# Optimization experiments

Measured on AMD Instinct MI355X. Metric: run time of the kernel, lower is better.

Reference implementation:

```python
import jax, jax.numpy as jnp
import numpy as np

N = 20000
E = 500000
NS = 128
NT = 128
BN_EPS = 1e-3
DIMS = [NS, 2 * NT, 4 * NT, 2 * NT, NT, NT]


def setup_inputs() -> dict:
    key = jax.random.key(0)
    ks = jax.random.split(key, 32)
    inp = {
        "x": jax.random.normal(ks[0], (N, NS), jnp.float32),
        "edge_index": jax.random.randint(ks[1], (2, E), 0, N),
        "edge_attr": jax.random.uniform(ks[2], (E,), jnp.float32),
    }
    for i in range(5):
        din, dout = DIMS[i], DIMS[i + 1]
        inp[f"W{i+1}"] = jax.random.normal(ks[3 + i], (din, dout), jnp.float32) * (1.0 / np.sqrt(din)).astype(np.float32)
        inp[f"b{i+1}"] = jnp.zeros((dout,), jnp.float32)
    for i in range(4):
        d = DIMS[i + 1]
        inp[f"g{i+1}"] = 1.0 + 0.1 * jax.random.normal(ks[10 + i], (d,), jnp.float32)
        inp[f"be{i+1}"] = 0.1 * jax.random.normal(ks[14 + i], (d,), jnp.float32)
        inp[f"m{i+1}"] = 0.1 * jax.random.normal(ks[18 + i], (d,), jnp.float32)
        inp[f"v{i+1}"] = jax.random.uniform(ks[22 + i], (d,), jnp.float32, minval=0.5, maxval=1.5)
    return inp


def gcn_norm(edge_index, edge_attr, n):
    # PyG gcn_norm with self-loops (fill value 1) and symmetric degree norm.
    loop = jnp.arange(n)
    row = jnp.concatenate([edge_index[0], loop])
    col = jnp.concatenate([edge_index[1], loop])
    w = jnp.concatenate([edge_attr, jnp.ones((n,), edge_attr.dtype)])
    deg = jax.ops.segment_sum(w, col, num_segments=n)
    dinv = jnp.where(deg > 0, jax.lax.rsqrt(deg), 0.0)
    return row, col, dinv[row] * w * dinv[col]


def gcn_conv(h, W, b, row, col, norm, n):
    # out[col] += norm * (h @ W)[row]; then add bias (PyG GCNConv).
    hw = h @ W
    agg = jax.ops.segment_sum(hw[row] * norm[:, None], col, num_segments=n)
    return agg + b


def bn_eval(h, g, be, m, v):
    return (h - m) * jax.lax.rsqrt(v + BN_EPS) * g + be


def reference(x, edge_index, edge_attr,
              W1, b1, W2, b2, W3, b3, W4, b4, W5, b5,
              g1, be1, m1, v1, g2, be2, m2, v2,
              g3, be3, m3, v3, g4, be4, m4, v4):
    n = x.shape[0]
    row, col, norm = gcn_norm(edge_index, edge_attr, n)  # cached=True: shared by all layers
    h = jax.nn.sigmoid(bn_eval(gcn_conv(x, W1, b1, row, col, norm, n), g1, be1, m1, v1))
    h = jax.nn.sigmoid(bn_eval(gcn_conv(h, W2, b2, row, col, norm, n), g2, be2, m2, v2))
    h = jax.nn.sigmoid(bn_eval(gcn_conv(h, W3, b3, row, col, norm, n), g3, be3, m3, v3))
    h = jax.nn.sigmoid(bn_eval(gcn_conv(h, W4, b4, row, col, norm, n), g4, be4, m4, v4))
    h = jax.nn.sigmoid(gcn_conv(h, W5, b5, row, col, norm, n))
    # dropout is identity in eval mode
    x11 = h.T @ h  # [NT, NT]
    x12 = 0.5 * (x11 + x11.T)
    return x12 - jnp.diag(jnp.diag(x12))
```

## Files before the change

kernel.cpp:

```cpp
#include <hip/hip_runtime.h>
#include <hip/hip_bf16.h>
#include <hip/hip_fp8.h>
#include <cstdint>
#include <cstddef>

typedef __hip_bfloat16 bf16;
typedef unsigned char fp8;
typedef __attribute__((ext_vector_type(8))) short short8;
typedef __attribute__((ext_vector_type(4))) float f32x4;
typedef __attribute__((ext_vector_type(2))) float f32x2;

#define NSF 128
#define BN_EPS 1e-3f
#define NR 4
#define SCK 2048


__global__ void zero_fill_kernel(int* __restrict__ fill, int total) {
    int i = blockIdx.x * blockDim.x + threadIdx.x;
    if (i < total) fill[i] = 0;
}

__global__ void passA_kernel(const int* __restrict__ ei, int* __restrict__ fill,
                             int* __restrict__ loc, int E, int n, int rsize) {
    int idx = blockIdx.x * blockDim.x + threadIdx.x;
    if (idx < E) {
        int r = ei[idx];
        int c = ei[E + idx];
        int slot = c * NR + r / rsize;
        loc[idx] = atomicAdd(&fill[slot], 1);
    } else if (idx < E + n) {
        int i = idx - E;
        int slot = i * NR + i / rsize;
        loc[idx] = atomicAdd(&fill[slot], 1);
    }
}


__global__ void scan1_kernel(const int* __restrict__ cnt, int* __restrict__ blksum, int total) {
    __shared__ int red[256];
    int base = blockIdx.x * SCK + threadIdx.x * 8;
    int s = 0;
    #pragma unroll
    for (int i = 0; i < 8; ++i) {
        int idx = base + i;
        if (idx < total) s += cnt[idx];
    }
    red[threadIdx.x] = s;
    __syncthreads();
    for (int off2 = 128; off2 > 0; off2 >>= 1) {
        if (threadIdx.x < off2) red[threadIdx.x] += red[threadIdx.x + off2];
        __syncthreads();
    }
    if (threadIdx.x == 0) blksum[blockIdx.x] = red[0];
}

__global__ void scan2_kernel(int* __restrict__ blksum, int* __restrict__ row_ptr,
                             int nblk, int total) {
    __shared__ int part[256];
    int tid = threadIdx.x;
    int v = (tid < nblk) ? blksum[tid] : 0;
    part[tid] = v;
    __syncthreads();
    for (int off2 = 1; off2 < 256; off2 <<= 1) {
        int t = (tid >= off2) ? part[tid - off2] : 0;
        __syncthreads();
        part[tid] += t;
        __syncthreads();
    }
    if (tid < nblk) blksum[tid] = part[tid] - v;
    if (tid == 255) row_ptr[total] = part[255];
}

__global__ void scan3_kernel(const int* __restrict__ cnt, const int* __restrict__ blkoff,
                             int* __restrict__ row_ptr, int total) {
    __shared__ int part[256];
    int tid = threadIdx.x;
    int base = blockIdx.x * SCK + tid * 8;
    int loc[8]; int s = 0;
    #pragma unroll
    for (int i = 0; i < 8; ++i) {
        int idx = base + i;
        loc[i] = (idx < total) ? cnt[idx] : 0;
        s += loc[i];
    }
    part[tid] = s;
    __syncthreads();
    for (int off2 = 1; off2 < 256; off2 <<= 1) {
        int t = (tid >= off2) ? part[tid - off2] : 0;
        __syncthreads();
        part[tid] += t;
        __syncthreads();
    }
    int run = blkoff[blockIdx.x] + part[tid] - s;
    #pragma unroll
    for (int i = 0; i < 8; ++i) {
        int idx = base + i;
        if (idx < total) { row_ptr[idx] = run; run += loc[i]; }
    }
}

__global__ void passB_kernel(const int* __restrict__ ei, const float* __restrict__ ea,
                             const int* __restrict__ row_ptr, const int* __restrict__ loc,
                             int2* __restrict__ e8, int* __restrict__ csr_col,
                             int E, int n, int rsize) {
    int idx = blockIdx.x * blockDim.x + threadIdx.x;
    if (idx < E) {
        int r = ei[idx];
        int c = ei[E + idx];
        int slot = c * NR + r / rsize;
        int p = row_ptr[slot] + loc[idx];
        int2 rec; rec.x = r; rec.y = __float_as_int(ea[idx]);
        e8[p] = rec;
        csr_col[p] = c;
    } else if (idx < E + n) {
        int i = idx - E;
        int slot = i * NR + i / rsize;
        int p = row_ptr[slot] + loc[idx];
        int2 rec; rec.x = i; rec.y = __float_as_int(1.0f);
        e8[p] = rec;
        csr_col[p] = i;
    }
}

__global__ void degdinv_kernel(const int* __restrict__ row_ptr, const int2* __restrict__ e8,
                               float* __restrict__ dinv, int n) {
    int node = blockIdx.x * blockDim.x + threadIdx.x;
    if (node < n) {
        int s = row_ptr[node * NR], e = row_ptr[(node + 1) * NR];
        float d = 0.0f;
        for (int j = s; j < e; ++j) d += __int_as_float(e8[j].y);
        dinv[node] = (d > 0.0f) ? rsqrtf(d) : 0.0f;
    }
}

__global__ void normw_kernel(const float* __restrict__ dinv, const int* __restrict__ csr_col,
                             int2* __restrict__ e8, int EN) {
    int p = blockIdx.x * blockDim.x + threadIdx.x;
    if (p < EN) {
        int2 rec = e8[p];
        float w = dinv[rec.x] * __int_as_float(rec.y) * dinv[csr_col[p]];
        ((int*)e8)[2 * p + 1] = __float_as_int(w);
    }
}


__device__ inline void store_val(bf16* C, size_t idx, float a) {
    C[idx] = __float2bfloat16(a);
}
__device__ inline void store_val(fp8* C, size_t idx, float a) {
    int packed = __builtin_amdgcn_cvt_pk_fp8_f32(a, a, 0, false);
    C[idx] = (fp8)(packed & 0xff);
}

__global__ void prep_kernel(const float* __restrict__ x, fp8* __restrict__ xq, int xcnt,
                            const float* __restrict__ W0, const float* __restrict__ W1,
                            const float* __restrict__ W2, const float* __restrict__ W3,
                            const float* __restrict__ W4,
                            bf16* __restrict__ wtbuf, int wtelems) {
    int idx = blockIdx.x * blockDim.x + threadIdx.x;
    if (idx < xcnt) {
        store_val(xq, idx, x[idx]);
        return;
    }
    int widx = idx - xcnt;
    if (widx >= wtelems) return;
    const float* W; int K, N, off;
    if (widx < 32768)       { W = W0; K = 128; N = 256; off = 0; }
    else if (widx < 163840) { W = W1; K = 256; N = 512; off = 32768; }
    else if (widx < 294912) { W = W2; K = 512; N = 256; off = 163840; }
    else if (widx < 327680) { W = W3; K = 256; N = 128; off = 294912; }
    else                    { W = W4; K = 128; N = 128; off = 327680; }
    int l = widx - off;
    int nn = l / K, kk = l % K;
    wtbuf[widx] = __float2bfloat16(W[(size_t)kk * N + nn]);
}


__device__ inline void gl_lds16(const bf16* g, bf16* l) {
    __builtin_amdgcn_global_load_lds(
        (const __attribute__((address_space(1))) void*)g,
        (__attribute__((address_space(3))) void*)l,
        16, 0, 0);
}


template <typename OT>
__global__ __launch_bounds__(256) void mfma_gemm_kernel(
    const bf16* __restrict__ A, const bf16* __restrict__ Wt,
    OT* __restrict__ C, int M, int K, int N, int mode,
    const float* __restrict__ bias, const float* __restrict__ g,
    const float* __restrict__ be, const float* __restrict__ m,
    const float* __restrict__ v) {
    __shared__ bf16 As[64][32];
    __shared__ bf16 Bs[128][32];
    int m0 = blockIdx.x * 64;
    int n0 = blockIdx.y * 128;
    int tid = threadIdx.x;
    int wave = tid >> 6, lane = tid & 63;
    int lrow = lane & 15, quad = lane >> 4;

    f32x4 acc[8] = {};

    int srow = lane >> 2;
    int sseg = lane & 3;
    int am = wave * 16 + srow;
    int bn = wave * 32 + srow;
    bool aok = (m0 + am) < M;

    for (int k0 = 0; k0 < K; k0 += 32) {
        if (aok)
            gl_lds16(A + (size_t)(m0 + am) * K + k0 + sseg * 8, &As[am][sseg * 8]);
        gl_lds16(Wt + (size_t)(n0 + bn) * K + k0 + sseg * 8, &Bs[bn][sseg * 8]);
        gl_lds16(Wt + (size_t)(n0 + bn + 16) * K + k0 + sseg * 8, &Bs[bn + 16][sseg * 8]);
        __syncthreads();

        short8 afrag = *(const short8*)(&As[wave * 16 + lrow][quad * 8]);
        #pragma unroll
        for (int t = 0; t < 8; ++t) {
            short8 bfrag = *(const short8*)(&Bs[t * 16 + lrow][quad * 8]);
            acc[t] = __builtin_amdgcn_mfma_f32_16x16x32_bf16(afrag, bfrag, acc[t], 0, 0, 0);
        }
        __syncthreads();
    }
    #pragma unroll
    for (int t = 0; t < 8; ++t) {
        int gn = n0 + t * 16 + lrow;
        float bsc = 0.0f, scale = 1.0f, mean = 0.0f, beta = 0.0f;
        if (mode == 1) {
            bsc = bias[gn];
            scale = g[gn] * rsqrtf(v[gn] + BN_EPS);
            mean = m[gn];
            beta = be[gn];
        }
        #pragma unroll
        for (int rr = 0; rr < 4; ++rr) {
            int gm = m0 + wave * 16 + quad * 4 + rr;
            if (gm < M) {
                float a = acc[t][rr];
                if (mode == 1) {
                    a = (a + bsc - mean) * scale + beta;
                    a = 1.0f / (1.0f + __expf(-a));
                }
                store_val(C, (size_t)gm * N + gn, a);
            }
        }
    }
}


template <int VEC> struct F8Vec;
template <> struct F8Vec<2> { typedef unsigned short T; };
template <> struct F8Vec<4> { typedef unsigned int T; };

__device__ inline void fma_f8(unsigned short q, float w, float* acc) {
    f32x2 lo = __builtin_amdgcn_cvt_pk_f32_fp8((unsigned int)q, false);
    acc[0] += w * lo.x;
    acc[1] += w * lo.y;
}
__device__ inline void fma_f8(unsigned int q, float w, float* acc) {
    f32x2 lo = __builtin_amdgcn_cvt_pk_f32_fp8(q, false);
    f32x2 hi = __builtin_amdgcn_cvt_pk_f32_fp8(q, true);
    acc[0] += w * lo.x;
    acc[1] += w * lo.y;
    acc[2] += w * hi.x;
    acc[3] += w * hi.y;
}

template <int VEC>
__global__ __launch_bounds__(256) void agg_fp8_kernel(
    const fp8* __restrict__ hw,
    const int* __restrict__ row_ptr, const int2* __restrict__ e8,
    const float* __restrict__ bias,
    const float* __restrict__ g, const float* __restrict__ be,
    const float* __restrict__ m, const float* __restrict__ v,
    bf16* __restrict__ out, int n, int mode) {
    typedef typename F8Vec<VEC>::T T;
    const int dfeat = VEC * 64;
    int wave = threadIdx.x >> 6;
    int lane = threadIdx.x & 63;
    int node = blockIdx.x * 4 + wave;
    if (node >= n) return;
    int s = row_ptr[node * NR], e = row_ptr[(node + 1) * NR];
    float acc[VEC];
    #pragma unroll
    for (int i = 0; i < VEC; ++i) acc[i] = 0.0f;
    const size_t base = (size_t)lane * VEC;

    int j = s;
    for (; j + 7 < e; j += 8) {
        int2 ew[8];
        #pragma unroll
        for (int u = 0; u < 8; ++u) ew[u] = e8[j + u];
        T q[8];
        #pragma unroll
        for (int u = 0; u < 8; ++u)
            q[u] = *(const T*)(hw + (size_t)ew[u].x * dfeat + base);
        #pragma unroll
        for (int u = 0; u < 8; ++u)
            fma_f8(q[u], __int_as_float(ew[u].y), acc);
    }
    for (; j + 3 < e; j += 4) {
        int2 ew[4];
        #pragma unroll
        for (int u = 0; u < 4; ++u) ew[u] = e8[j + u];
        T q[4];
        #pragma unroll
        for (int u = 0; u < 4; ++u)
            q[u] = *(const T*)(hw + (size_t)ew[u].x * dfeat + base);
        #pragma unroll
        for (int u = 0; u < 4; ++u)
            fma_f8(q[u], __int_as_float(ew[u].y), acc);
    }
    for (; j < e; ++j) {
        int2 ew = e8[j];
        T q = *(const T*)(hw + (size_t)ew.x * dfeat + base);
        fma_f8(q, __int_as_float(ew.y), acc);
    }

    #pragma unroll
    for (int i = 0; i < VEC; ++i) {
        int f = (int)base + i;
        float a = acc[i];
        if (mode != 0) {
            a += bias[f];
            if (mode == 1) {
                float scale = g[f] * rsqrtf(v[f] + BN_EPS);
                a = (a - m[f]) * scale + be[f];
            }
            a = 1.0f / (1.0f + __expf(-a));
        }
        out[(size_t)node * dfeat + f] = __float2bfloat16(a);
    }
}

#define TPAD 8

__global__ __launch_bounds__(256) void htht_mfma_kernel(
    const bf16* __restrict__ h, float* __restrict__ partial, int n) {
    __shared__ bf16 hsT[128][32 + TPAD];
    int b = blockIdx.x;
    int tid = threadIdx.x;
    int wave = tid >> 6, lane = tid & 63;
    int lrow = lane & 15, quad = lane >> 4;

    f32x4 acc[2][8] = {};

    int kk = tid >> 3;
    int seg = tid & 7;

    for (int kt = 0; kt < 8; ++kt) {
        int k0 = b * 256 + kt * 32;
        #pragma unroll
        for (int s2 = 0; s2 < 2; ++s2) {
            int fs = (seg + s2 * 8) * 8;
            int gk = k0 + kk;
            uint4 q; q.x = q.y = q.z = q.w = 0u;
            if (gk < n) q = *(const uint4*)(h + (size_t)gk * 128 + fs);
            const unsigned short* u = (const unsigned short*)&q;
            #pragma unroll
            for (int i = 0; i < 8; ++i)
                *((unsigned short*)&hsT[fs + i][kk]) = u[i];
        }
        __syncthreads();
        short8 af0 = *(const short8*)(&hsT[wave * 32 + lrow][quad * 8]);
        short8 af1 = *(const short8*)(&hsT[wave * 32 + 16 + lrow][quad * 8]);
        #pragma unroll
        for (int t = 0; t < 8; ++t) {
            short8 bfrag = *(const short8*)(&hsT[t * 16 + lrow][quad * 8]);
            acc[0][t] = __builtin_amdgcn_mfma_f32_16x16x32_bf16(af0, bfrag, acc[0][t], 0, 0, 0);
            acc[1][t] = __builtin_amdgcn_mfma_f32_16x16x32_bf16(af1, bfrag, acc[1][t], 0, 0, 0);
        }
        __syncthreads();
    }
    float* p = partial + (size_t)b * 16384;
    #pragma unroll
    for (int a_ = 0; a_ < 2; ++a_) {
        #pragma unroll
        for (int t = 0; t < 8; ++t) {
            #pragma unroll
            for (int rr = 0; rr < 4; ++rr) {
                int gm = wave * 32 + a_ * 16 + quad * 4 + rr;
                int gn = t * 16 + lrow;
                p[gm * 128 + gn] = acc[a_][t][rr];
            }
        }
    }
}

__global__ void reduce_kernel(const float* __restrict__ partial, float* __restrict__ out, int nchunks) {
    int idx = blockIdx.x * blockDim.x + threadIdx.x;
    float s = 0.0f;
    for (int c = 0; c < nchunks; ++c) s += partial[(size_t)c * 16384 + idx];
    int i = idx / 128, j = idx % 128;
    out[idx] = (i == j) ? 0.0f : s;
}

extern "C" void kernel_launch(void* const* d_in, const int* in_sizes, int n_in,
                              void* d_out, int out_size, void* d_ws, size_t ws_size,
                              hipStream_t stream) {
    const float* x  = (const float*)d_in[0];
    const int*   ei = (const int*)d_in[1];
    const float* ea = (const float*)d_in[2];
    const float* W[5];  const float* bvec[5];
    for (int l = 0; l < 5; ++l) { W[l] = (const float*)d_in[3 + 2 * l]; bvec[l] = (const float*)d_in[4 + 2 * l]; }
    const float* g[4]; const float* be[4]; const float* mm[4]; const float* vv[4];
    for (int l = 0; l < 4; ++l) {
        g[l]  = (const float*)d_in[13 + 4 * l];
        be[l] = (const float*)d_in[14 + 4 * l];
        mm[l] = (const float*)d_in[15 + 4 * l];
        vv[l] = (const float*)d_in[16 + 4 * l];
    }
    const int n = in_sizes[0] / NSF;
    const int E = in_sizes[1] / 2;
    const int EN = E + n;
    const int rsize = (n + NR - 1) / NR;
    const int total = n * NR;
    const int nscan = (total + SCK - 1) / SCK;
    const int dims[6] = {128, 256, 512, 256, 128, 128};
    const int wtoff[5] = {0, 32768, 163840, 294912, 327680};
    const int wtelems = 344064;

    auto align = [](size_t o) { return (o + 255) & ~(size_t)255; };
    size_t off = 0;
    float* dinv    = (float*)((char*)d_ws + off); off = align(off + (size_t)n * 4);
    int*   fill    = (int*)  ((char*)d_ws + off); off = align(off + (size_t)total * 4);
    int*   row_ptr = (int*)  ((char*)d_ws + off); off = align(off + ((size_t)total + 1) * 4);
    int*   blksum  = (int*)  ((char*)d_ws + off); off = align(off + (size_t)256 * 4);
    int*   locb    = (int*)  ((char*)d_ws + off); off = align(off + (size_t)EN * 4);
    int2*  e8      = (int2*) ((char*)d_ws + off); off = align(off + (size_t)EN * 8);
    int*   csr_col = (int*)  ((char*)d_ws + off); off = align(off + (size_t)EN * 4);
    bf16*  wtbuf   = (bf16*) ((char*)d_ws + off); off = align(off + (size_t)wtelems * 2);
    fp8*   xq      = (fp8*)  ((char*)d_ws + off); off = align(off + (size_t)n * 128);
    bf16*  hbuf    = (bf16*) ((char*)d_ws + off); off = align(off + (size_t)n * 512 * 2);
    bf16*  abuf    = (bf16*) ((char*)d_ws + off); off = align(off + (size_t)n * 512 * 2);
    fp8*   f8buf   = (fp8*)  ((char*)d_ws + off); off = align(off + (size_t)n * 256);
    const int KCH = (20000 + 255) / 256;
    float* partial = (float*)((char*)d_ws + off); off = align(off + (size_t)KCH * 16384 * 4);

    zero_fill_kernel<<<(total + 255) / 256, 256, 0, stream>>>(fill, total);
    passA_kernel<<<(EN + 255) / 256, 256, 0, stream>>>(ei, fill, locb, E, n, rsize);
    scan1_kernel<<<nscan, 256, 0, stream>>>(fill, blksum, total);
    scan2_kernel<<<1, 256, 0, stream>>>(blksum, row_ptr, nscan, total);
    scan3_kernel<<<nscan, 256, 0, stream>>>(fill, blksum, row_ptr, total);
    passB_kernel<<<(EN + 255) / 256, 256, 0, stream>>>(ei, ea, row_ptr, locb,
                                                       e8, csr_col, E, n, rsize);
    degdinv_kernel<<<(n + 255) / 256, 256, 0, stream>>>(row_ptr, e8, dinv, n);
    normw_kernel<<<(EN + 255) / 256, 256, 0, stream>>>(dinv, csr_col, e8, EN);

    {
        int xcnt = n * 128;
        int items = xcnt + wtelems;
        prep_kernel<<<(items + 255) / 256, 256, 0, stream>>>(x, xq, xcnt,
            W[0], W[1], W[2], W[3], W[4], wtbuf, wtelems);
    }

    int ablocks = (n + 3) / 4;
    auto gemm_bf16 = [&](const bf16* A, int l, bf16* C, int mode) {
        int K = dims[l], N = dims[l + 1];
        dim3 gg((n + 63) / 64, N / 128);
        int bi = (l < 4) ? l : 0;
        mfma_gemm_kernel<bf16><<<gg, 256, 0, stream>>>(A, wtbuf + wtoff[l], C, n, K, N, mode,
                                                       bvec[l], g[bi], be[bi], mm[bi], vv[bi]);
    };
    auto gemm_fp8 = [&](const bf16* A, int l, fp8* C, int mode) {
        int K = dims[l], N = dims[l + 1];
        dim3 gg((n + 63) / 64, N / 128);
        int bi = (l < 4) ? l : 0;
        mfma_gemm_kernel<fp8><<<gg, 256, 0, stream>>>(A, wtbuf + wtoff[l], C, n, K, N, mode,
                                                      bvec[l], g[bi], be[bi], mm[bi], vv[bi]);
    };

    agg_fp8_kernel<2><<<ablocks, 256, 0, stream>>>(xq, row_ptr, e8,
        bvec[0], bvec[0], bvec[0], bvec[0], bvec[0], abuf, n, 0);
    gemm_fp8(abuf, 0, f8buf, 1);
    agg_fp8_kernel<4><<<ablocks, 256, 0, stream>>>(f8buf, row_ptr, e8,
        bvec[1], bvec[1], bvec[1], bvec[1], bvec[1], abuf, n, 0);
    gemm_bf16(abuf, 1, hbuf, 1);
    gemm_fp8(hbuf, 2, f8buf, 0);
    agg_fp8_kernel<4><<<ablocks, 256, 0, stream>>>(f8buf, row_ptr, e8,
        bvec[2], g[2], be[2], mm[2], vv[2], abuf, n, 1);
    gemm_fp8(abuf, 3, f8buf, 0);
    agg_fp8_kernel<2><<<ablocks, 256, 0, stream>>>(f8buf, row_ptr, e8,
        bvec[3], g[3], be[3], mm[3], vv[3], hbuf, n, 1);
    gemm_fp8(hbuf, 4, f8buf, 0);
    agg_fp8_kernel<2><<<ablocks, 256, 0, stream>>>(f8buf, row_ptr, e8,
        bvec[4], bvec[4], bvec[4], bvec[4], bvec[4], abuf, n, 2);

    htht_mfma_kernel<<<KCH, 256, 0, stream>>>(abuf, partial, n);
    reduce_kernel<<<16384 / 256, 256, 0, stream>>>(partial, (float*)d_out, KCH);
}
```

Measured before the change: 408.1 us.

## Retile MFMA GEMM waves to 4x2 fragments and fold zero-fill into prep kernel

The GEMM kernel now has each wave cover all 64 rows and a 32-column slice, using 4 A fragments and 2 B fragments per k-step. Before, each wave covered 16 rows across all 128 columns. This cuts LDS fragment reads per MFMA from 9 per 8 to 6 per 8. Separately, the zero-fill of the CSR bucket counters moves into the prep kernel, removing one kernel launch. That means the weight and input conversion now runs before the graph-build passes instead of after them.

```diff
diff --git a/kernel.cpp b/kernel.cpp
--- a/kernel.cpp
+++ b/kernel.cpp
@@ -15,11 +15,6 @@
 #define NR 4
 #define SCK 2048
 
-
-__global__ void zero_fill_kernel(int* __restrict__ fill, int total) {
-    int i = blockIdx.x * blockDim.x + threadIdx.x;
-    if (i < total) fill[i] = 0;
-}
 
 __global__ void passA_kernel(const int* __restrict__ ei, int* __restrict__ fill,
                              int* __restrict__ loc, int E, int n, int rsize) {
@@ -153,27 +148,33 @@
     C[idx] = (fp8)(packed & 0xff);
 }
 
-__global__ void prep_kernel(const float* __restrict__ x, fp8* __restrict__ xq, int xcnt,
+__global__ void prep_kernel(int* __restrict__ fill, int total,
+                            const float* __restrict__ x, fp8* __restrict__ xq, int xcnt,
                             const float* __restrict__ W0, const float* __restrict__ W1,
                             const float* __restrict__ W2, const float* __restrict__ W3,
                             const float* __restrict__ W4,
                             bf16* __restrict__ wtbuf, int wtelems) {
     int idx = blockIdx.x * blockDim.x + threadIdx.x;
+    if (idx < total) { fill[idx] = 0; return; }
+    idx -= total;
     if (idx < xcnt) {
         store_val(xq, idx, x[idx]);
         return;
     }
     int widx = idx - xcnt;
     if (widx >= wtelems) return;
-    const float* W; int K, N, off;
-    if (widx < 32768)       { W = W0; K = 128; N = 256; off = 0; }
-    else if (widx < 163840) { W = W1; K = 256; N = 512; off = 32768; }
-    else if (widx < 294912) { W = W2; K = 512; N = 256; off = 163840; }
-    else if (widx < 327680) { W = W3; K = 256; N = 128; off = 294912; }
-    else                    { W = W4; K = 128; N = 128; off = 327680; }
+    const float* W; int K, off;
+    if (widx < 32768)       { W = W0; K = 128; off = 0; }
+    else if (widx < 163840) { W = W1; K = 256; off = 32768; }
+    else if (widx < 294912) { W = W2; K = 512; off = 163840; }
+    else if (widx < 327680) { W = W3; K = 256; off = 294912; }
+    else                    { W = W4; K = 128; off = 327680; }
+    int N2;
+    if (widx < 32768) N2 = 256; else if (widx < 163840) N2 = 512;
+    else if (widx < 294912) N2 = 256; else N2 = 128;
     int l = widx - off;
     int nn = l / K, kk = l % K;
-    wtbuf[widx] = __float2bfloat16(W[(size_t)kk * N + nn]);
+    wtbuf[widx] = __float2bfloat16(W[(size_t)kk * N2 + nn]);
 }
 
 
@@ -200,7 +201,7 @@
     int wave = tid >> 6, lane = tid & 63;
     int lrow = lane & 15, quad = lane >> 4;
 
-    f32x4 acc[8] = {};
+    f32x4 acc[4][2] = {};
 
     int srow = lane >> 2;
     int sseg = lane & 3;
@@ -215,17 +216,24 @@
         gl_lds16(Wt + (size_t)(n0 + bn + 16) * K + k0 + sseg * 8, &Bs[bn + 16][sseg * 8]);
         __syncthreads();
 
-        short8 afrag = *(const short8*)(&As[wave * 16 + lrow][quad * 8]);
-        #pragma unroll
-        for (int t = 0; t < 8; ++t) {
-            short8 bfrag = *(const short8*)(&Bs[t * 16 + lrow][quad * 8]);
-            acc[t] = __builtin_amdgcn_mfma_f32_16x16x32_bf16(afrag, bfrag, acc[t], 0, 0, 0);
-        }
-        __syncthreads();
-    }
-    #pragma unroll
-    for (int t = 0; t < 8; ++t) {
-        int gn = n0 + t * 16 + lrow;
+        short8 afrag[4], bfrag[2];
+        #pragma unroll
+        for (int mt = 0; mt < 4; ++mt)
+            afrag[mt] = *(const short8*)(&As[mt * 16 + lrow][quad * 8]);
+        #pragma unroll
+        for (int nt = 0; nt < 2; ++nt)
+            bfrag[nt] = *(const short8*)(&Bs[wave * 32 + nt * 16 + lrow][quad * 8]);
+        #pragma unroll
+        for (int mt = 0; mt < 4; ++mt)
+            #pragma unroll
+            for (int nt = 0; nt < 2; ++nt)
+                acc[mt][nt] = __builtin_amdgcn_mfma_f32_16x16x32_bf16(
+                    afrag[mt], bfrag[nt], acc[mt][nt], 0, 0, 0);
+        __syncthreads();
+    }
+    #pragma unroll
+    for (int nt = 0; nt < 2; ++nt) {
+        int gn = n0 + wave * 32 + nt * 16 + lrow;
         float bsc = 0.0f, scale = 1.0f, mean = 0.0f, beta = 0.0f;
         if (mode == 1) {
             bsc = bias[gn];
@@ -234,15 +242,18 @@
             beta = be[gn];
         }
         #pragma unroll
-        for (int rr = 0; rr < 4; ++rr) {
-            int gm = m0 + wave * 16 + quad * 4 + rr;
-            if (gm < M) {
-                float a = acc[t][rr];
-                if (mode == 1) {
-                    a = (a + bsc - mean) * scale + beta;
-                    a = 1.0f / (1.0f + __expf(-a));
+        for (int mt = 0; mt < 4; ++mt) {
+            #pragma unroll
+            for (int rr = 0; rr < 4; ++rr) {
+                int gm = m0 + mt * 16 + quad * 4 + rr;
+                if (gm < M) {
+                    float a = acc[mt][nt][rr];
+                    if (mode == 1) {
+                        a = (a + bsc - mean) * scale + beta;
+                        a = 1.0f / (1.0f + __expf(-a));
+                    }
+                    store_val(C, (size_t)gm * N + gn, a);
                 }
-                store_val(C, (size_t)gm * N + gn, a);
             }
         }
     }
@@ -438,7 +449,13 @@
     const int KCH = (20000 + 255) / 256;
     float* partial = (float*)((char*)d_ws + off); off = align(off + (size_t)KCH * 16384 * 4);
 
-    zero_fill_kernel<<<(total + 255) / 256, 256, 0, stream>>>(fill, total);
+    {
+        int xcnt = n * 128;
+        int items = total + xcnt + wtelems;
+        prep_kernel<<<(items + 255) / 256, 256, 0, stream>>>(fill, total, x, xq, xcnt,
+            W[0], W[1], W[2], W[3], W[4], wtbuf, wtelems);
+    }
+
     passA_kernel<<<(EN + 255) / 256, 256, 0, stream>>>(ei, fill, locb, E, n, rsize);
     scan1_kernel<<<nscan, 256, 0, stream>>>(fill, blksum, total);
     scan2_kernel<<<1, 256, 0, stream>>>(blksum, row_ptr, nscan, total);
@@ -447,13 +464,6 @@
                                                        e8, csr_col, E, n, rsize);
     degdinv_kernel<<<(n + 255) / 256, 256, 0, stream>>>(row_ptr, e8, dinv, n);
     normw_kernel<<<(EN + 255) / 256, 256, 0, stream>>>(dinv, csr_col, e8, EN);
-
-    {
-        int xcnt = n * 128;
-        int items = xcnt + wtelems;
-        prep_kernel<<<(items + 255) / 256, 256, 0, stream>>>(x, xq, xcnt,
-            W[0], W[1], W[2], W[3], W[4], wtbuf, wtelems);
-    }
 
     int ablocks = (n + 3) / 4;
     auto gemm_bf16 = [&](const bf16* A, int l, bf16* C, int mode) {
```

New measurement: 400.4 us. About the same (-1.9%).
